# Performance work log

Hardware: AMD Instinct MI355X
Metric: run time of the kernel (lower is better)

Reference implementation:

```python
import jax, jax.numpy as jnp
import numpy as np

N, K, D = 65536, 8192, 512
EPS_NORM = 1e-12  # F.normalize clamp eps


def setup_inputs() -> dict:
    key = jax.random.key(0)
    k1, k2 = jax.random.split(key)
    z = jax.random.normal(k1, (N, D), dtype=jnp.float32)
    embedding = jax.random.normal(k2, (K, D), dtype=jnp.float32)  # learned codebook param
    return {"z": z, "embedding": embedding}


def reference(z, embedding):
    # L2-normalize inputs and codebook rows (F.normalize semantics: x / max(||x||, eps))
    zn = z / jnp.maximum(jnp.linalg.norm(z, axis=-1, keepdims=True), EPS_NORM)          # [N, D]
    cb = embedding / jnp.maximum(jnp.linalg.norm(embedding, axis=-1, keepdims=True), EPS_NORM)  # [K, D]
    # squared euclidean distances: ||z||^2 - 2 z.c + ||c||^2  -> [N, K]
    d = (jnp.sum(zn * zn, axis=1, keepdims=True)
         - 2.0 * jnp.einsum('nd,kd->nk', zn, cb)
         + jnp.sum(cb * cb, axis=1))
    indices = jnp.argmin(d, axis=1)          # [N] int
    z_q = cb[indices]                        # [N, D] gather of nearest codes
    # projection of z onto its quantized code direction
    z_proj = jnp.sum(zn * z_q, axis=1, keepdims=True) * z_q  # [N, D]
    return z_proj, indices
```

## Files before the change

kernel.cpp:

```cpp
#include <hip/hip_runtime.h>
#include <stdint.h>

#define N_ROWS 65536
#define K_CODES 8192
#define D_DIM 512
#define EPS_NORM 1e-12f
#define NB 64
#define MARGIN 2.5e-3f
#define CAP 16

typedef _Float16 f16x8 __attribute__((ext_vector_type(8)));
typedef _Float16 f16x4 __attribute__((ext_vector_type(4)));
typedef float f32x4 __attribute__((ext_vector_type(4)));
typedef unsigned long long u64;

__device__ __forceinline__ unsigned orderf(float f) {
  unsigned u = __float_as_uint(f);
  return (u & 0x80000000u) ? ~u : (u | 0x80000000u);
}
__device__ __forceinline__ float unorderf(unsigned ub) {
  unsigned u = (ub & 0x80000000u) ? (ub & 0x7FFFFFFFu) : ~ub;
  return __uint_as_float(u);
}
__device__ __forceinline__ unsigned umin32(unsigned a, unsigned b) { return a < b ? a : b; }
__device__ __forceinline__ u64 umin64(u64 a, u64 b) { return a < b ? a : b; }
__device__ __forceinline__ u64 shfl_xor_u64(u64 v, int m) {
  unsigned lo = (unsigned)__shfl_xor((int)(unsigned)(v & 0xFFFFFFFFull), m, 64);
  unsigned hi = (unsigned)__shfl_xor((int)(unsigned)(v >> 32), m, 64);
  return ((u64)hi << 32) | (u64)lo;
}
__device__ __forceinline__ void async_copy16(void* lds, const void* g) {
  __builtin_amdgcn_global_load_lds(
      (const __attribute__((address_space(1))) void*)g,
      (__attribute__((address_space(3))) void*)lds, 16, 0, 0);
}

__global__ __launch_bounds__(256) void prep_z_kernel(
    const float* __restrict__ z, _Float16* __restrict__ znh,
    float* __restrict__ znorm, float* __restrict__ znorm2) {
  const int row = blockIdx.x * 4 + ((int)threadIdx.x >> 6);
  const int lane = (int)threadIdx.x & 63;
  const float4* xr = (const float4*)(z + (size_t)row * D_DIM);
  float4 v0 = xr[lane];
  float4 v1 = xr[lane + 64];
  float ss = v0.x * v0.x + v0.y * v0.y + v0.z * v0.z + v0.w * v0.w
           + v1.x * v1.x + v1.y * v1.y + v1.z * v1.z + v1.w * v1.w;
#pragma unroll
  for (int s = 32; s > 0; s >>= 1) ss += __shfl_xor(ss, s, 64);
  const float m = fmaxf(sqrtf(ss), EPS_NORM);
  const float rm = 1.0f / m;
  float4 o0, o1;
  o0.x = v0.x * rm; o0.y = v0.y * rm; o0.z = v0.z * rm; o0.w = v0.w * rm;
  o1.x = v1.x * rm; o1.y = v1.y * rm; o1.z = v1.z * rm; o1.w = v1.w * rm;
  float s2 = o0.x * o0.x + o0.y * o0.y + o0.z * o0.z + o0.w * o0.w
           + o1.x * o1.x + o1.y * o1.y + o1.z * o1.z + o1.w * o1.w;
#pragma unroll
  for (int s = 32; s > 0; s >>= 1) s2 += __shfl_xor(s2, s, 64);
  f16x4 h0, h1;
  h0[0] = (_Float16)o0.x; h0[1] = (_Float16)o0.y; h0[2] = (_Float16)o0.z; h0[3] = (_Float16)o0.w;
  h1[0] = (_Float16)o1.x; h1[1] = (_Float16)o1.y; h1[2] = (_Float16)o1.z; h1[3] = (_Float16)o1.w;
  *(f16x4*)(znh + (size_t)row * D_DIM + lane * 4) = h0;
  *(f16x4*)(znh + (size_t)row * D_DIM + 256 + lane * 4) = h1;
  if (lane == 0) { znorm[row] = m; znorm2[row] = s2; }
}

__global__ __launch_bounds__(256) void prep_cb_kernel(
    const float* __restrict__ emb, float* __restrict__ cb32,
    _Float16* __restrict__ cbh, float* __restrict__ cnorm2,
    unsigned* __restrict__ counters) {
  if (blockIdx.x == 0 && threadIdx.x < 2) counters[threadIdx.x] = 0;
  const int row = blockIdx.x * 4 + ((int)threadIdx.x >> 6);
  const int lane = (int)threadIdx.x & 63;
  const float4* xr = (const float4*)(emb + (size_t)row * D_DIM);
  float4 v0 = xr[lane];
  float4 v1 = xr[lane + 64];
  float ss = v0.x * v0.x + v0.y * v0.y + v0.z * v0.z + v0.w * v0.w
           + v1.x * v1.x + v1.y * v1.y + v1.z * v1.z + v1.w * v1.w;
#pragma unroll
  for (int s = 32; s > 0; s >>= 1) ss += __shfl_xor(ss, s, 64);
  const float m = fmaxf(sqrtf(ss), EPS_NORM);
  float4 o0, o1;
  o0.x = v0.x / m; o0.y = v0.y / m; o0.z = v0.z / m; o0.w = v0.w / m;
  o1.x = v1.x / m; o1.y = v1.y / m; o1.z = v1.z / m; o1.w = v1.w / m;
  float s2 = o0.x * o0.x + o0.y * o0.y + o0.z * o0.z + o0.w * o0.w
           + o1.x * o1.x + o1.y * o1.y + o1.z * o1.z + o1.w * o1.w;
#pragma unroll
  for (int s = 32; s > 0; s >>= 1) s2 += __shfl_xor(s2, s, 64);
  float4* co = (float4*)(cb32 + (size_t)row * D_DIM);
  co[lane] = o0;
  co[lane + 64] = o1;
  f16x4 h0, h1;
  h0[0] = (_Float16)o0.x; h0[1] = (_Float16)o0.y; h0[2] = (_Float16)o0.z; h0[3] = (_Float16)o0.w;
  h1[0] = (_Float16)o1.x; h1[1] = (_Float16)o1.y; h1[2] = (_Float16)o1.z; h1[3] = (_Float16)o1.w;
  *(f16x4*)(cbh + (size_t)row * D_DIM + lane * 4) = h0;
  *(f16x4*)(cbh + (size_t)row * D_DIM + 256 + lane * 4) = h1;
  if (lane == 0) cnorm2[row] = s2;
}

#define LGKM0 asm volatile("s_waitcnt lgkmcnt(0)" ::: "memory")
#define VM4 asm volatile("s_waitcnt vmcnt(4)" ::: "memory")
#define VM0 asm volatile("s_waitcnt vmcnt(0)" ::: "memory")
#define BARF                                                                  \
  do { asm volatile("" ::: "memory"); __builtin_amdgcn_s_barrier();           \
       asm volatile("" ::: "memory"); } while (0)

#define STAGE(b, kt)                                                          \
  do {                                                                        \
    async_copy16(lds + (b) * 8192 + tid * 8,        gZ  + (kt) * 32);         \
    async_copy16(lds + (b) * 8192 + 2048 + tid * 8, gZ2 + (kt) * 32);         \
    async_copy16(lds + (b) * 8192 + 4096 + tid * 8, gC  + (kt) * 32);         \
    async_copy16(lds + (b) * 8192 + 6144 + tid * 8, gC2 + (kt) * 32);         \
  } while (0)

#define COMPUTE(b)                                                            \
  do {                                                                        \
    f16x8 zF[4], cF[4];                                                       \
    _Pragma("unroll") for (int mf_ = 0; mf_ < 4; ++mf_)                       \
      zF[mf_] = *(const f16x8*)(zRd + (b) * 8192 + mf_ * 512);                \
    _Pragma("unroll") for (int nf_ = 0; nf_ < 4; ++nf_)                       \
      cF[nf_] = *(const f16x8*)(cRd + (b) * 8192 + nf_ * 512);                \
    LGKM0;                                                                    \
    __builtin_amdgcn_sched_barrier(0);                                        \
    _Pragma("unroll") for (int nf_ = 0; nf_ < 4; ++nf_)                       \
      _Pragma("unroll") for (int mf_ = 0; mf_ < 4; ++mf_)                     \
        acc[nf_][mf_] = __builtin_amdgcn_mfma_f32_16x16x32_f16(               \
            cF[nf_], zF[mf_], acc[nf_][mf_], 0, 0, 0);                        \
  } while (0)

__global__ __launch_bounds__(256, 3) void screen_gemm_kernel(
    const _Float16* __restrict__ znh, const _Float16* __restrict__ cbh,
    u64* __restrict__ K1, unsigned* __restrict__ K2) {
  __shared__ __align__(16) _Float16 lds[24576];
  const int tid = (int)threadIdx.x;
  const int lane = tid & 63;
  const int wv = tid >> 6;
  const int wm = wv >> 1;
  const int wn = wv & 1;
  const int q = lane >> 4;
  const int c15 = lane & 15;

  const int o = (int)blockIdx.x;
  const int jb = o >> 3;
  const int bx = (o & 7) * 8 + (jb & 7);
  const int by = jb >> 3;
  const int m0 = by * 128;
  const int n0 = bx * 128;

  const int srow = tid >> 2;
  const int sch = (tid & 3) ^ ((tid >> 3) & 3);
  const _Float16* gZ  = znh + (size_t)(m0 + srow) * D_DIM + sch * 8;
  const _Float16* gZ2 = gZ + (size_t)64 * D_DIM;
  const _Float16* gC  = cbh + (size_t)(n0 + srow) * D_DIM + sch * 8;
  const _Float16* gC2 = gC + (size_t)64 * D_DIM;

  const int rk = (q ^ ((c15 >> 1) & 3)) * 8;
  const _Float16* zRd = lds + (wm * 64 + c15) * 32 + rk;
  const _Float16* cRd = lds + 4096 + (wn * 64 + c15) * 32 + rk;

  f32x4 acc[4][4];
  const f32x4 z4 = {0.0f, 0.0f, 0.0f, 0.0f};
#pragma unroll
  for (int i = 0; i < 4; i++)
#pragma unroll
    for (int jj = 0; jj < 4; jj++) acc[i][jj] = z4;

  STAGE(0, 0); STAGE(1, 1);
  VM4; BARF;
  STAGE(2, 2);  COMPUTE(0); VM4; BARF;
  STAGE(0, 3);  COMPUTE(1); VM4; BARF;
  STAGE(1, 4);  COMPUTE(2); VM4; BARF;
  STAGE(2, 5);  COMPUTE(0); VM4; BARF;
  STAGE(0, 6);  COMPUTE(1); VM4; BARF;
  STAGE(1, 7);  COMPUTE(2); VM4; BARF;
  STAGE(2, 8);  COMPUTE(0); VM4; BARF;
  STAGE(0, 9);  COMPUTE(1); VM4; BARF;
  STAGE(1, 10); COMPUTE(2); VM4; BARF;
  STAGE(2, 11); COMPUTE(0); VM4; BARF;
  STAGE(0, 12); COMPUTE(1); VM4; BARF;
  STAGE(1, 13); COMPUTE(2); VM4; BARF;
  STAGE(2, 14); COMPUTE(0); VM4; BARF;
  STAGE(0, 15); COMPUTE(1); VM4; BARF;
  COMPUTE(2); VM0; BARF;
  COMPUTE(0);

  __syncthreads();
  u64* kbuf = (u64*)lds;
  unsigned* vbuf = (unsigned*)(lds + 1024);
#pragma unroll
  for (int mf = 0; mf < 4; ++mf) {
    float v1 = __builtin_inff(), v2 = __builtin_inff();
    int c1 = 0;
#pragma unroll
    for (int nf = 0; nf < 4; ++nf)
#pragma unroll
      for (int r = 0; r < 4; ++r) {
        float v = -acc[nf][mf][r];
        int col = n0 + wn * 64 + nf * 16 + q * 4 + r;
        if (v < v1) { v2 = v1; v1 = v; c1 = col; }
        else        { v2 = fminf(v2, v); }
      }
    u64 key1 = ((u64)orderf(v1) << 32) | (u64)(unsigned)c1;
    unsigned b2 = orderf(v2);
#pragma unroll
    for (int s = 16; s <= 32; s <<= 1) {
      u64 ok = shfl_xor_u64(key1, s);
      unsigned ob2 = (unsigned)__shfl_xor((int)b2, s, 64);
      unsigned ov = (unsigned)(ok >> 32);
      unsigned v1k = (unsigned)(key1 >> 32);
      unsigned lose = (ok < key1) ? v1k : ov;
      b2 = umin32(umin32(b2, ob2), lose);
      key1 = umin64(key1, ok);
    }
    if (q == 0) {
      const int rowL = wm * 64 + mf * 16 + c15;
      kbuf[rowL * 2 + wn] = key1;
      vbuf[rowL * 2 + wn] = b2;
    }
  }
  __syncthreads();
  if (tid < 128) {
    u64 k0 = kbuf[tid * 2], k1v = kbuf[tid * 2 + 1];
    unsigned v0 = vbuf[tid * 2], v1 = vbuf[tid * 2 + 1];
    u64 kk = umin64(k0, k1v);
    unsigned lose = (k0 < k1v) ? (unsigned)(k1v >> 32) : (unsigned)(k0 >> 32);
    unsigned t2 = umin32(umin32(v0, v1), lose);
    const size_t oo = (size_t)(m0 + tid) * NB + bx;
    K1[oo] = kk;
    K2[oo] = t2;
  }
}

__global__ __launch_bounds__(256) void certify_kernel(
    const u64* __restrict__ K1, const unsigned* __restrict__ K2,
    unsigned* __restrict__ idx_final, unsigned* __restrict__ candList,
    unsigned* __restrict__ candCount, unsigned* __restrict__ lightList,
    unsigned* __restrict__ heavyList, unsigned* __restrict__ counters) {
  const int row = blockIdx.x * 4 + (int)(threadIdx.x >> 6);
  const int b = (int)(threadIdx.x & 63);
  u64 k = K1[(size_t)row * NB + b];
  unsigned t2 = K2[(size_t)row * NB + b];
  u64 kmin = k;
#pragma unroll
  for (int s = 1; s <= 32; s <<= 1) kmin = umin64(kmin, shfl_xor_u64(kmin, s));
  const float t1f = unorderf((unsigned)(kmin >> 32));
  const unsigned thr = orderf(t1f + MARGIN);
  const bool cand = ((unsigned)(k >> 32)) <= thr;
  const bool heavy = (t2 <= thr);
  u64 cmask = __ballot(cand);
  u64 hmask = __ballot(heavy);
  const int nc = __popcll(cmask);
  if (hmask != 0 || nc > CAP) {
    if (b == 0) {
      unsigned p = atomicAdd(counters + 1, 1u);
      heavyList[p] = (unsigned)row;
    }
  } else if (nc == 1) {
    if (b == 0) idx_final[row] = (unsigned)(kmin & 0xFFFFFFFFull);
  } else {
    if (cand) {
      int pos = __popcll(cmask & ((b == 0) ? 0ull : (~0ull >> (64 - b))));
      candList[(size_t)row * CAP + pos] = (unsigned)(k & 0xFFFFFFFFull);
    }
    if (b == 0) {
      candCount[row] = (unsigned)nc;
      unsigned p = atomicAdd(counters + 0, 1u);
      lightList[p] = (unsigned)row;
    }
  }
}

__global__ __launch_bounds__(64) void rescore_light_kernel(
    const float* __restrict__ z, const float* __restrict__ cb32,
    const float* __restrict__ znorm, const float* __restrict__ znorm2,
    const float* __restrict__ cnorm2, const unsigned* __restrict__ candList,
    const unsigned* __restrict__ candCount,
    const unsigned* __restrict__ lightList,
    const unsigned* __restrict__ counters, unsigned* __restrict__ idx_final) {
  const int lane = (int)threadIdx.x;
  const unsigned n = counters[0];
  for (unsigned i = blockIdx.x; i < n; i += gridDim.x) {
    const int row = (int)lightList[i];
    const float m = znorm[row];
    const float zn2 = znorm2[row];
    const float4* zr = (const float4*)(z + (size_t)row * D_DIM);
    float4 v0 = zr[lane], v1 = zr[lane + 64];
    float4 o0, o1;
    o0.x = v0.x / m; o0.y = v0.y / m; o0.z = v0.z / m; o0.w = v0.w / m;
    o1.x = v1.x / m; o1.y = v1.y / m; o1.z = v1.z / m; o1.w = v1.w / m;
    const unsigned nc = candCount[row];
    u64 best = ~0ull;
    for (unsigned j = 0; j < nc; j++) {
      const unsigned c = candList[(size_t)row * CAP + j];
      const float4* qr = (const float4*)(cb32 + (size_t)c * D_DIM);
      float4 q0 = qr[lane], q1 = qr[lane + 64];
      float p = o0.x * q0.x + o0.y * q0.y + o0.z * q0.z + o0.w * q0.w
              + o1.x * q1.x + o1.y * q1.y + o1.z * q1.z + o1.w * q1.w;
#pragma unroll
      for (int s = 32; s > 0; s >>= 1) p += __shfl_xor(p, s, 64);
      float dist = __fadd_rn(__fsub_rn(zn2, __fmul_rn(2.0f, p)), cnorm2[c]);
      u64 key = ((u64)orderf(dist) << 32) | (u64)c;
      best = umin64(best, key);
    }
    if (lane == 0) idx_final[row] = (unsigned)(best & 0xFFFFFFFFull);
  }
}

__global__ __launch_bounds__(64) void rescore_heavy_kernel(
    const float* __restrict__ z, const float* __restrict__ cb32,
    const float* __restrict__ znorm, const float* __restrict__ znorm2,
    const float* __restrict__ cnorm2, const u64* __restrict__ K1,
    const unsigned* __restrict__ heavyList,
    const unsigned* __restrict__ counters, unsigned* __restrict__ idx_final) {
  __shared__ float znl[D_DIM];
  const int lane = (int)threadIdx.x;
  const unsigned n = counters[1];
  for (unsigned i = blockIdx.x; i < n; i += gridDim.x) {
    const int row = (int)heavyList[i];
    const float m = znorm[row];
    const float4* zr = (const float4*)(z + (size_t)row * D_DIM);
    float4 v0 = zr[lane], v1 = zr[lane + 64];
    __syncthreads();
    float4 o0, o1;
    o0.x = v0.x / m; o0.y = v0.y / m; o0.z = v0.z / m; o0.w = v0.w / m;
    o1.x = v1.x / m; o1.y = v1.y / m; o1.z = v1.z / m; o1.w = v1.w / m;
    *(float4*)&znl[lane * 4] = o0;
    *(float4*)&znl[256 + lane * 4] = o1;
    u64 k = K1[(size_t)row * NB + lane];
    u64 kmin = k;
#pragma unroll
    for (int s = 1; s <= 32; s <<= 1) kmin = umin64(kmin, shfl_xor_u64(kmin, s));
    const float t1 = unorderf((unsigned)(kmin >> 32));
    const bool cf = unorderf((unsigned)(k >> 32)) <= t1 + MARGIN;
    u64 mask = __ballot(cf);
    __syncthreads();
    const float zn2 = znorm2[row];
    u64 best = ~0ull;
    while (mask) {
      const int b = __builtin_ctzll(mask);
      mask &= mask - 1;
#pragma unroll
      for (int h = 0; h < 2; h++) {
        const int c = b * 128 + h * 64 + lane;
        const float4* cr = (const float4*)(cb32 + (size_t)c * D_DIM);
        float dot = 0.0f;
        for (int d = 0; d < 128; d++) {
          float4 bb = cr[d];
          float4 aa = *(const float4*)&znl[d * 4];
          dot = __fmaf_rn(aa.x, bb.x, dot);
          dot = __fmaf_rn(aa.y, bb.y, dot);
          dot = __fmaf_rn(aa.z, bb.z, dot);
          dot = __fmaf_rn(aa.w, bb.w, dot);
        }
        float dist = __fadd_rn(__fsub_rn(zn2, __fmul_rn(2.0f, dot)), cnorm2[c]);
        u64 key = ((u64)orderf(dist) << 32) | (u64)(unsigned)c;
        best = umin64(best, key);
      }
    }
#pragma unroll
    for (int s = 1; s <= 32; s <<= 1) best = umin64(best, shfl_xor_u64(best, s));
    if (lane == 0) idx_final[row] = (unsigned)(best & 0xFFFFFFFFull);
  }
}

__global__ __launch_bounds__(256) void finalize_kernel(
    const float* __restrict__ z, const float* __restrict__ cb32,
    const float* __restrict__ znorm, const unsigned* __restrict__ idx_final,
    float* __restrict__ out) {
  const int row = blockIdx.x * 4 + ((int)threadIdx.x >> 6);
  const int lane = (int)threadIdx.x & 63;
  const float m = znorm[row];
  const unsigned idx = idx_final[row];
  const float4* zr = (const float4*)(z + (size_t)row * D_DIM);
  const float4* qr = (const float4*)(cb32 + (size_t)idx * D_DIM);
  float4 v0 = zr[lane], v1 = zr[lane + 64];
  float4 q0 = qr[lane], q1 = qr[lane + 64];
  float4 z0, z1;
  z0.x = v0.x / m; z0.y = v0.y / m; z0.z = v0.z / m; z0.w = v0.w / m;
  z1.x = v1.x / m; z1.y = v1.y / m; z1.z = v1.z / m; z1.w = v1.w / m;
  float p = z0.x * q0.x + z0.y * q0.y + z0.z * q0.z + z0.w * q0.w
          + z1.x * q1.x + z1.y * q1.y + z1.z * q1.z + z1.w * q1.w;
#pragma unroll
  for (int s = 32; s > 0; s >>= 1) p += __shfl_xor(p, s, 64);
  float4 o0, o1;
  o0.x = p * q0.x; o0.y = p * q0.y; o0.z = p * q0.z; o0.w = p * q0.w;
  o1.x = p * q1.x; o1.y = p * q1.y; o1.z = p * q1.z; o1.w = p * q1.w;
  float4* orow = (float4*)(out + (size_t)row * D_DIM);
  orow[lane] = o0;
  orow[lane + 64] = o1;
  if (lane == 0) out[(size_t)N_ROWS * D_DIM + row] = (float)idx;
}

extern "C" void kernel_launch(void* const* d_in, const int* in_sizes, int n_in,
                              void* d_out, int out_size, void* d_ws,
                              size_t ws_size, hipStream_t stream) {
  const float* z = (const float*)d_in[0];
  const float* emb = (const float*)d_in[1];
  float* out = (float*)d_out;

  u64* K1 = (u64*)d_ws;
  unsigned* K2 = (unsigned*)(K1 + (size_t)N_ROWS * NB);
  float* cb32 = (float*)(K2 + (size_t)N_ROWS * NB);
  float* znorm = cb32 + (size_t)K_CODES * D_DIM;
  float* znorm2 = znorm + N_ROWS;
  float* cnorm2 = znorm2 + N_ROWS;
  unsigned* idx_final = (unsigned*)(cnorm2 + K_CODES);
  unsigned* lightList = idx_final + N_ROWS;
  unsigned* heavyList = lightList + N_ROWS;
  unsigned* candCount = heavyList + N_ROWS;
  unsigned* counters = candCount + N_ROWS;
  unsigned* candList = counters + 64;
  _Float16* znh = (_Float16*)(candList + (size_t)N_ROWS * CAP);
  _Float16* cbh = znh + (size_t)N_ROWS * D_DIM;

  prep_z_kernel<<<N_ROWS / 4, 256, 0, stream>>>(z, znh, znorm, znorm2);
  prep_cb_kernel<<<K_CODES / 4, 256, 0, stream>>>(emb, cb32, cbh, cnorm2,
                                                  counters);

  screen_gemm_kernel<<<32768, 256, 0, stream>>>(znh, cbh, K1, K2);

  certify_kernel<<<N_ROWS / 4, 256, 0, stream>>>(
      K1, K2, idx_final, candList, candCount, lightList, heavyList, counters);
  rescore_light_kernel<<<8192, 64, 0, stream>>>(
      z, cb32, znorm, znorm2, cnorm2, candList, candCount, lightList, counters,
      idx_final);
  rescore_heavy_kernel<<<512, 64, 0, stream>>>(
      z, cb32, znorm, znorm2, cnorm2, K1, heavyList, counters, idx_final);
  finalize_kernel<<<N_ROWS / 4, 256, 0, stream>>>(z, cb32, znorm, idx_final,
                                                  out);
}
```

Baseline: 1.239 ms.

## Fuse certify, light/heavy rescore and finalize into a single resolve kernel

Replaces the four post-GEMM kernels (certify with atomic work lists, light rescore, heavy rescore, finalize) with one kernel where each wavefront certifies its row, rescores candidates or does an exact fp32 scan of heavy buckets, then writes the projection. This removes three launches, the candidate and work-list buffers, the atomics, and the repeated reads of z and znorm. The cost is that heavy rows now run inline inside a 256-thread block, so divergent heavy work can stall its block and leave load imbalance where the old persistent heavy kernel spread it out. The heavy path also drops the old CAP overflow route, so rows with many candidates are now rescored exactly on the light path.

```diff
diff --git a/kernel.cpp b/kernel.cpp
--- a/kernel.cpp
+++ b/kernel.cpp
@@ -7,7 +7,6 @@
 #define EPS_NORM 1e-12f
 #define NB 64
 #define MARGIN 2.5e-3f
-#define CAP 16
 
 typedef _Float16 f16x8 __attribute__((ext_vector_type(8)));
 typedef _Float16 f16x4 __attribute__((ext_vector_type(4)));
@@ -66,9 +65,7 @@
 
 __global__ __launch_bounds__(256) void prep_cb_kernel(
     const float* __restrict__ emb, float* __restrict__ cb32,
-    _Float16* __restrict__ cbh, float* __restrict__ cnorm2,
-    unsigned* __restrict__ counters) {
-  if (blockIdx.x == 0 && threadIdx.x < 2) counters[threadIdx.x] = 0;
+    _Float16* __restrict__ cbh, float* __restrict__ cnorm2) {
   const int row = blockIdx.x * 4 + ((int)threadIdx.x >> 6);
   const int lane = (int)threadIdx.x & 63;
   const float4* xr = (const float4*)(emb + (size_t)row * D_DIM);
@@ -230,15 +227,18 @@
   }
 }
 
-__global__ __launch_bounds__(256) void certify_kernel(
-    const u64* __restrict__ K1, const unsigned* __restrict__ K2,
-    unsigned* __restrict__ idx_final, unsigned* __restrict__ candList,
-    unsigned* __restrict__ candCount, unsigned* __restrict__ lightList,
-    unsigned* __restrict__ heavyList, unsigned* __restrict__ counters) {
-  const int row = blockIdx.x * 4 + (int)(threadIdx.x >> 6);
-  const int b = (int)(threadIdx.x & 63);
-  u64 k = K1[(size_t)row * NB + b];
-  unsigned t2 = K2[(size_t)row * NB + b];
+__global__ __launch_bounds__(256) void resolve_kernel(
+    const float* __restrict__ z, const float* __restrict__ cb32,
+    const float* __restrict__ znorm, const float* __restrict__ znorm2,
+    const float* __restrict__ cnorm2, const u64* __restrict__ K1,
+    const unsigned* __restrict__ K2, float* __restrict__ out) {
+  __shared__ float znl[4][D_DIM];
+  const int w = (int)threadIdx.x >> 6;
+  const int lane = (int)threadIdx.x & 63;
+  const int row = (int)blockIdx.x * 4 + w;
+
+  u64 k = K1[(size_t)row * NB + lane];
+  unsigned t2 = K2[(size_t)row * NB + lane];
   u64 kmin = k;
 #pragma unroll
   for (int s = 1; s <= 32; s <<= 1) kmin = umin64(kmin, shfl_xor_u64(kmin, s));
@@ -248,49 +248,26 @@
   const bool heavy = (t2 <= thr);
   u64 cmask = __ballot(cand);
   u64 hmask = __ballot(heavy);
-  const int nc = __popcll(cmask);
-  if (hmask != 0 || nc > CAP) {
-    if (b == 0) {
-      unsigned p = atomicAdd(counters + 1, 1u);
-      heavyList[p] = (unsigned)row;
-    }
-  } else if (nc == 1) {
-    if (b == 0) idx_final[row] = (unsigned)(kmin & 0xFFFFFFFFull);
-  } else {
-    if (cand) {
-      int pos = __popcll(cmask & ((b == 0) ? 0ull : (~0ull >> (64 - b))));
-      candList[(size_t)row * CAP + pos] = (unsigned)(k & 0xFFFFFFFFull);
-    }
-    if (b == 0) {
-      candCount[row] = (unsigned)nc;
-      unsigned p = atomicAdd(counters + 0, 1u);
-      lightList[p] = (unsigned)row;
-    }
-  }
-}
-
-__global__ __launch_bounds__(64) void rescore_light_kernel(
-    const float* __restrict__ z, const float* __restrict__ cb32,
-    const float* __restrict__ znorm, const float* __restrict__ znorm2,
-    const float* __restrict__ cnorm2, const unsigned* __restrict__ candList,
-    const unsigned* __restrict__ candCount,
-    const unsigned* __restrict__ lightList,
-    const unsigned* __restrict__ counters, unsigned* __restrict__ idx_final) {
-  const int lane = (int)threadIdx.x;
-  const unsigned n = counters[0];
-  for (unsigned i = blockIdx.x; i < n; i += gridDim.x) {
-    const int row = (int)lightList[i];
-    const float m = znorm[row];
+
+  const float m = znorm[row];
+  const float4* zr = (const float4*)(z + (size_t)row * D_DIM);
+  float4 v0 = zr[lane], v1 = zr[lane + 64];
+  float4 o0, o1;
+  o0.x = v0.x / m; o0.y = v0.y / m; o0.z = v0.z / m; o0.w = v0.w / m;
+  o1.x = v1.x / m; o1.y = v1.y / m; o1.z = v1.z / m; o1.w = v1.w / m;
+
+  unsigned idx;
+  if (hmask == 0 && __popcll(cmask) == 1) {
+    idx = (unsigned)(kmin & 0xFFFFFFFFull);
+  } else if (hmask == 0) {
     const float zn2 = znorm2[row];
-    const float4* zr = (const float4*)(z + (size_t)row * D_DIM);
-    float4 v0 = zr[lane], v1 = zr[lane + 64];
-    float4 o0, o1;
-    o0.x = v0.x / m; o0.y = v0.y / m; o0.z = v0.z / m; o0.w = v0.w / m;
-    o1.x = v1.x / m; o1.y = v1.y / m; o1.z = v1.z / m; o1.w = v1.w / m;
-    const unsigned nc = candCount[row];
     u64 best = ~0ull;
-    for (unsigned j = 0; j < nc; j++) {
-      const unsigned c = candList[(size_t)row * CAP + j];
+    u64 mm = cmask;
+    while (mm) {
+      const int b = __builtin_ctzll(mm);
+      mm &= mm - 1;
+      const unsigned c =
+          (unsigned)__shfl((int)(unsigned)(k & 0xFFFFFFFFull), b, 64);
       const float4* qr = (const float4*)(cb32 + (size_t)c * D_DIM);
       float4 q0 = qr[lane], q1 = qr[lane + 64];
       float p = o0.x * q0.x + o0.y * q0.y + o0.z * q0.z + o0.w * q0.w
@@ -301,43 +278,16 @@
       u64 key = ((u64)orderf(dist) << 32) | (u64)c;
       best = umin64(best, key);
     }
-    if (lane == 0) idx_final[row] = (unsigned)(best & 0xFFFFFFFFull);
-  }
-}
-
-__global__ __launch_bounds__(64) void rescore_heavy_kernel(
-    const float* __restrict__ z, const float* __restrict__ cb32,
-    const float* __restrict__ znorm, const float* __restrict__ znorm2,
-    const float* __restrict__ cnorm2, const u64* __restrict__ K1,
-    const unsigned* __restrict__ heavyList,
-    const unsigned* __restrict__ counters, unsigned* __restrict__ idx_final) {
-  __shared__ float znl[D_DIM];
-  const int lane = (int)threadIdx.x;
-  const unsigned n = counters[1];
-  for (unsigned i = blockIdx.x; i < n; i += gridDim.x) {
-    const int row = (int)heavyList[i];
-    const float m = znorm[row];
-    const float4* zr = (const float4*)(z + (size_t)row * D_DIM);
-    float4 v0 = zr[lane], v1 = zr[lane + 64];
-    __syncthreads();
-    float4 o0, o1;
-    o0.x = v0.x / m; o0.y = v0.y / m; o0.z = v0.z / m; o0.w = v0.w / m;
-    o1.x = v1.x / m; o1.y = v1.y / m; o1.z = v1.z / m; o1.w = v1.w / m;
-    *(float4*)&znl[lane * 4] = o0;
-    *(float4*)&znl[256 + lane * 4] = o1;
-    u64 k = K1[(size_t)row * NB + lane];
-    u64 kmin = k;
-#pragma unroll
-    for (int s = 1; s <= 32; s <<= 1) kmin = umin64(kmin, shfl_xor_u64(kmin, s));
-    const float t1 = unorderf((unsigned)(kmin >> 32));
-    const bool cf = unorderf((unsigned)(k >> 32)) <= t1 + MARGIN;
-    u64 mask = __ballot(cf);
-    __syncthreads();
+    idx = (unsigned)(best & 0xFFFFFFFFull);
+  } else {
+    *(float4*)&znl[w][lane * 4] = o0;
+    *(float4*)&znl[w][256 + lane * 4] = o1;
     const float zn2 = znorm2[row];
     u64 best = ~0ull;
-    while (mask) {
-      const int b = __builtin_ctzll(mask);
-      mask &= mask - 1;
+    u64 mm = cmask;
+    while (mm) {
+      const int b = __builtin_ctzll(mm);
+      mm &= mm - 1;
 #pragma unroll
       for (int h = 0; h < 2; h++) {
         const int c = b * 128 + h * 64 + lane;
@@ -345,7 +295,7 @@
         float dot = 0.0f;
         for (int d = 0; d < 128; d++) {
           float4 bb = cr[d];
-          float4 aa = *(const float4*)&znl[d * 4];
+          float4 aa = *(const float4*)&znl[w][d * 4];
           dot = __fmaf_rn(aa.x, bb.x, dot);
           dot = __fmaf_rn(aa.y, bb.y, dot);
           dot = __fmaf_rn(aa.z, bb.z, dot);
@@ -358,35 +308,21 @@
     }
 #pragma unroll
     for (int s = 1; s <= 32; s <<= 1) best = umin64(best, shfl_xor_u64(best, s));
-    if (lane == 0) idx_final[row] = (unsigned)(best & 0xFFFFFFFFull);
+    idx = (unsigned)(best & 0xFFFFFFFFull);
   }
-}
-
-__global__ __launch_bounds__(256) void finalize_kernel(
-    const float* __restrict__ z, const float* __restrict__ cb32,
-    const float* __restrict__ znorm, const unsigned* __restrict__ idx_final,
-    float* __restrict__ out) {
-  const int row = blockIdx.x * 4 + ((int)threadIdx.x >> 6);
-  const int lane = (int)threadIdx.x & 63;
-  const float m = znorm[row];
-  const unsigned idx = idx_final[row];
-  const float4* zr = (const float4*)(z + (size_t)row * D_DIM);
+
   const float4* qr = (const float4*)(cb32 + (size_t)idx * D_DIM);
-  float4 v0 = zr[lane], v1 = zr[lane + 64];
   float4 q0 = qr[lane], q1 = qr[lane + 64];
-  float4 z0, z1;
-  z0.x = v0.x / m; z0.y = v0.y / m; z0.z = v0.z / m; z0.w = v0.w / m;
-  z1.x = v1.x / m; z1.y = v1.y / m; z1.z = v1.z / m; z1.w = v1.w / m;
-  float p = z0.x * q0.x + z0.y * q0.y + z0.z * q0.z + z0.w * q0.w
-          + z1.x * q1.x + z1.y * q1.y + z1.z * q1.z + z1.w * q1.w;
+  float p = o0.x * q0.x + o0.y * q0.y + o0.z * q0.z + o0.w * q0.w
+          + o1.x * q1.x + o1.y * q1.y + o1.z * q1.z + o1.w * q1.w;
 #pragma unroll
   for (int s = 32; s > 0; s >>= 1) p += __shfl_xor(p, s, 64);
-  float4 o0, o1;
-  o0.x = p * q0.x; o0.y = p * q0.y; o0.z = p * q0.z; o0.w = p * q0.w;
-  o1.x = p * q1.x; o1.y = p * q1.y; o1.z = p * q1.z; o1.w = p * q1.w;
+  float4 r0, r1;
+  r0.x = p * q0.x; r0.y = p * q0.y; r0.z = p * q0.z; r0.w = p * q0.w;
+  r1.x = p * q1.x; r1.y = p * q1.y; r1.z = p * q1.z; r1.w = p * q1.w;
   float4* orow = (float4*)(out + (size_t)row * D_DIM);
-  orow[lane] = o0;
-  orow[lane + 64] = o1;
+  orow[lane] = r0;
+  orow[lane + 64] = r1;
   if (lane == 0) out[(size_t)N_ROWS * D_DIM + row] = (float)idx;
 }
 
@@ -403,28 +339,14 @@
   float* znorm = cb32 + (size_t)K_CODES * D_DIM;
   float* znorm2 = znorm + N_ROWS;
   float* cnorm2 = znorm2 + N_ROWS;
-  unsigned* idx_final = (unsigned*)(cnorm2 + K_CODES);
-  unsigned* lightList = idx_final + N_ROWS;
-  unsigned* heavyList = lightList + N_ROWS;
-  unsigned* candCount = heavyList + N_ROWS;
-  unsigned* counters = candCount + N_ROWS;
-  unsigned* candList = counters + 64;
-  _Float16* znh = (_Float16*)(candList + (size_t)N_ROWS * CAP);
+  _Float16* znh = (_Float16*)(cnorm2 + K_CODES);
   _Float16* cbh = znh + (size_t)N_ROWS * D_DIM;
 
   prep_z_kernel<<<N_ROWS / 4, 256, 0, stream>>>(z, znh, znorm, znorm2);
-  prep_cb_kernel<<<K_CODES / 4, 256, 0, stream>>>(emb, cb32, cbh, cnorm2,
-                                                  counters);
+  prep_cb_kernel<<<K_CODES / 4, 256, 0, stream>>>(emb, cb32, cbh, cnorm2);
 
   screen_gemm_kernel<<<32768, 256, 0, stream>>>(znh, cbh, K1, K2);
 
-  certify_kernel<<<N_ROWS / 4, 256, 0, stream>>>(
-      K1, K2, idx_final, candList, candCount, lightList, heavyList, counters);
-  rescore_light_kernel<<<8192, 64, 0, stream>>>(
-      z, cb32, znorm, znorm2, cnorm2, candList, candCount, lightList, counters,
-      idx_final);
-  rescore_heavy_kernel<<<512, 64, 0, stream>>>(
-      z, cb32, znorm, znorm2, cnorm2, K1, heavyList, counters, idx_final);
-  finalize_kernel<<<N_ROWS / 4, 256, 0, stream>>>(z, cb32, znorm, idx_final,
-                                                  out);
-}
+  resolve_kernel<<<N_ROWS / 4, 256, 0, stream>>>(
+      z, cb32, znorm, znorm2, cnorm2, K1, K2, out);
+}
```

New measurement: 1.085 ms. -12.4%, faster.
